# Kernel optimization log

Measured on AMD Instinct MI355X. Metric: run time of the kernel, lower is better.

Reference implementation:

```python
import jax, jax.numpy as jnp
import numpy as np

B, L, H, NH = 8, 256, 128, 4
D = H // NH
NEG = jnp.float32(-(2.0 ** 32) + 1.0)


def setup_inputs() -> dict:
    key = jax.random.key(0)
    ks = jax.random.split(key, 12)
    f = lambda k, s, sc=1.0: jax.random.normal(k, s, dtype=jnp.float32) * sc
    inp = {
        "queries": f(ks[0], (B, L, H)),
        "keys": f(ks[1], (B, L, H)),
        "time_matrix_K": f(ks[2], (B, L, L, H), 0.05),
        "time_matrix_V": f(ks[3], (B, L, L, H), 0.05),
        "abs_pos_K": f(ks[4], (B, L, H), 0.1),
        "abs_pos_V": f(ks[5], (B, L, H), 0.1),
        "Wq": f(ks[6], (H, H), 1.0 / np.sqrt(H)),
        "bq": jnp.zeros((H,), jnp.float32),
        "Wk": f(ks[7], (H, H), 1.0 / np.sqrt(H)),
        "bk": jnp.zeros((H,), jnp.float32),
        "Wv": f(ks[8], (H, H), 1.0 / np.sqrt(H)),
        "bv": jnp.zeros((H,), jnp.float32),
        # True = padded query row (masked out)
        "time_mask": jax.random.uniform(ks[9], (B, L)) < 0.1,
        # causal mask: True above the diagonal = not attendable
        "attn_mask": jnp.triu(jnp.ones((L, L), dtype=bool), k=1),
    }
    return inp


def reference(queries, keys, time_matrix_K, time_matrix_V, abs_pos_K, abs_pos_V,
              Wq, bq, Wk, bk, Wv, bv, time_mask, attn_mask):
    # Linear projections (torch Linear: x @ W.T + b)
    Q = queries @ Wq.T + bq
    K = keys @ Wk.T + bk
    V = keys @ Wv.T + bv
    # head split: channels [i*D:(i+1)*D] -> head i  (equivalent to torch split/cat)
    Qh = Q.reshape(B, L, NH, D)
    Kh = K.reshape(B, L, NH, D)
    Vh = V.reshape(B, L, NH, D)
    pKh = abs_pos_K.reshape(B, L, NH, D)
    pVh = abs_pos_V.reshape(B, L, NH, D)
    tKh = time_matrix_K.reshape(B, L, L, NH, D)
    tVh = time_matrix_V.reshape(B, L, L, NH, D)
    # scores: QK^T + Q*absposK^T + per-row time-interval bias  -> [B,NH,L,L]
    aw = jnp.einsum('blhd,bmhd->bhlm', Qh, Kh)
    aw += jnp.einsum('blhd,bmhd->bhlm', Qh, pKh)
    aw += jnp.einsum('blmhd,blhd->bhlm', tKh, Qh)
    aw = aw * jnp.float32(1.0 / np.sqrt(D))
    mask = time_mask[:, None, :, None] | attn_mask[None, None, :, :]
    aw = jnp.where(mask, NEG, aw)
    A = jax.nn.softmax(aw, axis=-1)  # dropout omitted (eval mode)
    # outputs: A@V + A@absposV + per-row A @ time_matrix_V  -> [B,L,NH,D]
    out = jnp.einsum('bhlm,bmhd->blhd', A, Vh)
    out += jnp.einsum('bhlm,bmhd->blhd', A, pVh)
    out += jnp.einsum('bhlm,blmhd->blhd', A, tVh)
    return out.reshape(B, L, H)
```

## Files before the change

kernel.cpp:

```cpp
#include <hip/hip_runtime.h>
#include <math.h>

#define Bdim 8
#define Lq   256
#define Hd   128

static constexpr float kNEG = -4294967295.0f;
static constexpr float kScale = 0.17677669529663687f;
static constexpr float kUni = 0.00390625f;

typedef float f32x4 __attribute__((ext_vector_type(4)));

__global__ __launch_bounds__(256) void prep_kernel(
    const float* __restrict__ Wq, const float* __restrict__ Wk,
    const float* __restrict__ Wv, const unsigned char* __restrict__ raw,
    float* __restrict__ Wt, int* __restrict__ outmask)
{
    const int blk = blockIdx.x;
    if (blk < 12) {
        __shared__ float tile[64][65];
        const int mi = blk >> 2;
        const float* W = (mi == 0) ? Wq : (mi == 1) ? Wk : Wv;
        float* WT = Wt + mi * (Hd * Hd);
        const int ti = blk & 3;
        const int r0 = (ti >> 1) * 64, c0 = (ti & 1) * 64;
        #pragma unroll
        for (int k = 0; k < 16; ++k) {
            const int e = threadIdx.x + k * 256;
            const int r = e >> 6, c = e & 63;
            tile[r][c] = W[(r0 + r) * Hd + (c0 + c)];
        }
        __syncthreads();
        #pragma unroll
        for (int k = 0; k < 16; ++k) {
            const int e = threadIdx.x + k * 256;
            const int r = e >> 6, c = e & 63;
            WT[(c0 + r) * Hd + (r0 + c)] = tile[c][r];
        }
    } else {
        __shared__ int cnt;
        if (threadIdx.x == 0) cnt = 0;
        __syncthreads();
        const int n = Bdim * Lq;
        for (int i = threadIdx.x; i < n; i += 256)
            if ((i & 3) && raw[i]) atomicAdd(&cnt, 1);
        __syncthreads();
        const bool is_u8 = (cnt > 0);
        const int* raw32 = (const int*)raw;
        for (int i = threadIdx.x; i < n; i += 256) {
            const int v = is_u8 ? (int)raw[i] : raw32[i];
            outmask[i] = (v != 0) ? 1 : 0;
        }
    }
}

__global__ __launch_bounds__(512) void proj_kernel(
    const float* __restrict__ queries, const float* __restrict__ keys,
    const float* __restrict__ absK, const float* __restrict__ absV,
    const float* __restrict__ Wt,
    const float* __restrict__ bq, const float* __restrict__ bk,
    const float* __restrict__ bv,
    float* __restrict__ Qb, float* __restrict__ Kb, float* __restrict__ Vb)
{
    constexpr int R = 8;
    __shared__ float xq[R][Hd];
    __shared__ float xk[R][Hd];
    const int row0 = blockIdx.x * R;
    const int tid = threadIdx.x;
    #pragma unroll
    for (int k = 0; k < 2; ++k) {
        const int e = tid + k * 512;
        const int r = e >> 7, c = e & 127;
        xq[r][c] = queries[(row0 + r) * Hd + c];
        xk[r][c] = keys[(row0 + r) * Hd + c];
    }
    __syncthreads();

    const int o = tid & 127, rh = tid >> 7;
    const int r0 = rh * 2, r1 = rh * 2 + 1;
    const float* __restrict__ Wtq = Wt;
    const float* __restrict__ Wtk = Wt + Hd * Hd;
    const float* __restrict__ Wtv = Wt + 2 * Hd * Hd;

    float qa0 = bq[o], qa1 = qa0;
    float ka0 = bk[o] + absK[(row0 + r0) * Hd + o];
    float ka1 = bk[o] + absK[(row0 + r1) * Hd + o];
    float va0 = bv[o] + absV[(row0 + r0) * Hd + o];
    float va1 = bv[o] + absV[(row0 + r1) * Hd + o];

    #pragma unroll 4
    for (int i = 0; i < Hd; ++i) {
        const float wq = Wtq[i * Hd + o];
        const float wk = Wtk[i * Hd + o];
        const float wv = Wtv[i * Hd + o];
        const float x0 = xq[r0][i], x1 = xq[r1][i];
        const float y0 = xk[r0][i], y1 = xk[r1][i];
        qa0 += x0 * wq; qa1 += x1 * wq;
        ka0 += y0 * wk; ka1 += y1 * wk;
        va0 += y0 * wv; va1 += y1 * wv;
    }
    Qb[(row0 + r0) * Hd + o] = qa0;  Qb[(row0 + r1) * Hd + o] = qa1;
    Kb[(row0 + r0) * Hd + o] = ka0;  Kb[(row0 + r1) * Hd + o] = ka1;
    Vb[(row0 + r0) * Hd + o] = va0;  Vb[(row0 + r1) * Hd + o] = va1;
}

__global__ __launch_bounds__(256) void attn_kernel(
    const float* __restrict__ Qb, const float* __restrict__ Kb,
    const float* __restrict__ Vb,
    const float* __restrict__ tK, const float* __restrict__ tV,
    const int* __restrict__ tmask, float* __restrict__ out)
{
    const int bid = blockIdx.x;
    const int b = bid & 7;
    const int p = bid >> 3;
    const int tid = threadIdx.x;
    const int h = tid >> 6;
    const int lane = tid & 63;
    const int m_off = (lane >> 2) & 15;
    const int cg = lane & 3;
    const int ch = h * 32 + cg * 8;

    const int ls[4] = {p, 127 - p, 128 + p, 255 - p};

    f32x4 q[4][2];
    const float* tKp[4];
    const float* tVp[4];
    bool  mk[4];
    int   n1[4], n2[4];
    int NT1 = 0, NT2 = 0;
    #pragma unroll
    for (int i = 0; i < 4; ++i) {
        const size_t row = ((size_t)b * Lq + ls[i]) * Hd;
        q[i][0] = *(const f32x4*)(Qb + row + ch) * kScale;
        q[i][1] = *(const f32x4*)(Qb + row + ch + 4) * kScale;
        tKp[i] = tK + row * Lq + (size_t)m_off * Hd + ch;
        tVp[i] = tV + row * Lq + (size_t)m_off * Hd + ch;
        mk[i] = (tmask[b * Lq + ls[i]] != 0);
        const int nt = (ls[i] >> 4) + 1;
        n1[i] = mk[i] ? 0 : nt;
        n2[i] = mk[i] ? 16 : nt;
        NT1 = (n1[i] > NT1) ? n1[i] : NT1;
        NT2 = (n2[i] > NT2) ? n2[i] : NT2;
    }
    const float* kpt = Kb + (size_t)b * Lq * Hd + (size_t)m_off * Hd + ch;
    const float* vpt = Vb + (size_t)b * Lq * Hd + (size_t)m_off * Hd + ch;

    float s[4][16];
    #pragma unroll
    for (int i = 0; i < 4; ++i)
        #pragma unroll
        for (int t = 0; t < 16; ++t) s[i][t] = kNEG;

    #pragma unroll
    for (int t = 0; t < 16; ++t) {
        if (t < NT1) {
            const f32x4 ka = *(const f32x4*)(kpt + t * 2048);
            const f32x4 kb = *(const f32x4*)(kpt + t * 2048 + 4);
            const int m = t * 16 + m_off;
            #pragma unroll
            for (int i = 0; i < 4; ++i) {
                if (t < n1[i]) {
                    const f32x4 sa = ka + *(const f32x4*)(tKp[i] + t * 2048);
                    const f32x4 sb = kb + *(const f32x4*)(tKp[i] + t * 2048 + 4);
                    float pp = q[i][0].x*sa.x + q[i][0].y*sa.y
                             + q[i][0].z*sa.z + q[i][0].w*sa.w
                             + q[i][1].x*sb.x + q[i][1].y*sb.y
                             + q[i][1].z*sb.z + q[i][1].w*sb.w;
                    pp += __shfl_xor(pp, 1);
                    pp += __shfl_xor(pp, 2);
                    s[i][t] = (m <= ls[i]) ? pp : kNEG;
                }
            }
        }
    }

    #pragma unroll
    for (int i = 0; i < 4; ++i) {
        if (!mk[i]) {
            float mx = s[i][0];
            #pragma unroll
            for (int t = 1; t < 16; ++t) mx = fmaxf(mx, s[i][t]);
            #pragma unroll
            for (int d = 4; d < 64; d <<= 1) mx = fmaxf(mx, __shfl_xor(mx, d));
            float sum = 0.f;
            #pragma unroll
            for (int t = 0; t < 16; ++t) { s[i][t] = expf(s[i][t] - mx); sum += s[i][t]; }
            #pragma unroll
            for (int d = 4; d < 64; d <<= 1) sum += __shfl_xor(sum, d);
            const float inv = 1.0f / sum;
            #pragma unroll
            for (int t = 0; t < 16; ++t) s[i][t] *= inv;
        } else {
            #pragma unroll
            for (int t = 0; t < 16; ++t) s[i][t] = kUni;
        }
    }

    f32x4 acc[4][2];
    #pragma unroll
    for (int i = 0; i < 4; ++i) { acc[i][0] = (f32x4){0,0,0,0}; acc[i][1] = (f32x4){0,0,0,0}; }

    #pragma unroll
    for (int t = 0; t < 16; ++t) {
        if (t < NT2) {
            const f32x4 va = *(const f32x4*)(vpt + t * 2048);
            const f32x4 vb = *(const f32x4*)(vpt + t * 2048 + 4);
            #pragma unroll
            for (int i = 0; i < 4; ++i) {
                if (t < n2[i]) {
                    const f32x4 ta = *(const f32x4*)(tVp[i] + t * 2048);
                    const f32x4 tb = *(const f32x4*)(tVp[i] + t * 2048 + 4);
                    acc[i][0] += s[i][t] * (va + ta);
                    acc[i][1] += s[i][t] * (vb + tb);
                }
            }
        }
    }
    #pragma unroll
    for (int i = 0; i < 4; ++i) {
        #pragma unroll
        for (int d = 4; d < 64; d <<= 1) {
            acc[i][0].x += __shfl_xor(acc[i][0].x, d);
            acc[i][0].y += __shfl_xor(acc[i][0].y, d);
            acc[i][0].z += __shfl_xor(acc[i][0].z, d);
            acc[i][0].w += __shfl_xor(acc[i][0].w, d);
            acc[i][1].x += __shfl_xor(acc[i][1].x, d);
            acc[i][1].y += __shfl_xor(acc[i][1].y, d);
            acc[i][1].z += __shfl_xor(acc[i][1].z, d);
            acc[i][1].w += __shfl_xor(acc[i][1].w, d);
        }
    }
    if (m_off == 0) {
        #pragma unroll
        for (int i = 0; i < 4; ++i) {
            float* o = out + ((size_t)b * Lq + ls[i]) * Hd + ch;
            *(f32x4*)o       = acc[i][0];
            *(f32x4*)(o + 4) = acc[i][1];
        }
    }
}

extern "C" void kernel_launch(void* const* d_in, const int* in_sizes, int n_in,
                              void* d_out, int out_size, void* d_ws, size_t ws_size,
                              hipStream_t stream) {
    const float* queries = (const float*)d_in[0];
    const float* keys    = (const float*)d_in[1];
    const float* tK      = (const float*)d_in[2];
    const float* tV      = (const float*)d_in[3];
    const float* absK    = (const float*)d_in[4];
    const float* absV    = (const float*)d_in[5];
    const float* Wq      = (const float*)d_in[6];
    const float* bq      = (const float*)d_in[7];
    const float* Wk      = (const float*)d_in[8];
    const float* bk      = (const float*)d_in[9];
    const float* Wv      = (const float*)d_in[10];
    const float* bv      = (const float*)d_in[11];
    const unsigned char* tmask_raw = (const unsigned char*)d_in[12];

    float* outp = (float*)d_out;

    const int rows = Bdim * Lq;
    float* Qb = (float*)d_ws;
    float* Kb = Qb + (size_t)rows * Hd;
    float* Vb = Kb + (size_t)rows * Hd;
    int* tmask = (int*)(Vb + (size_t)rows * Hd);
    float* Wt = (float*)(tmask + rows);

    prep_kernel<<<13, 256, 0, stream>>>(Wq, Wk, Wv, tmask_raw, Wt, tmask);
    proj_kernel<<<rows / 8, 512, 0, stream>>>(queries, keys, absK, absV, Wt,
                                              bq, bk, bv, Qb, Kb, Vb);
    attn_kernel<<<512, 256, 0, stream>>>(Qb, Kb, Vb, tK, tV, tmask, outp);
}
```

Measured before the change: 89.61 us.

## Split attention work so each wave handles one query row and head

Each wave previously handled four query rows for one head, which let it reuse the K/V loads across rows. Now a block's four waves cover two heads times two query rows (p and 255-p, chosen to balance the causal load), and the grid grows from 512 to 2048 blocks. A launch-bounds occupancy hint is added. The change cuts per-thread register use and per-wave serial work and gives more blocks for latency hiding, but K/V rows are reloaded per query row, though those loads are small next to the tK/tV streams.

```diff
diff --git a/kernel.cpp b/kernel.cpp
--- a/kernel.cpp
+++ b/kernel.cpp
@@ -104,139 +104,103 @@
     Vb[(row0 + r0) * Hd + o] = va0;  Vb[(row0 + r1) * Hd + o] = va1;
 }
 
-__global__ __launch_bounds__(256) void attn_kernel(
+__global__ __launch_bounds__(256, 6) void attn_kernel(
     const float* __restrict__ Qb, const float* __restrict__ Kb,
     const float* __restrict__ Vb,
     const float* __restrict__ tK, const float* __restrict__ tV,
     const int* __restrict__ tmask, float* __restrict__ out)
 {
     const int bid = blockIdx.x;
-    const int b = bid & 7;
-    const int p = bid >> 3;
+    const int b  = bid & 7;
+    const int hp = (bid >> 3) & 1;
+    const int p  = bid >> 4;
+
     const int tid = threadIdx.x;
-    const int h = tid >> 6;
+    const int w = tid >> 6;
     const int lane = tid & 63;
+    const int h = hp * 2 + (w & 1);
+    const int li = ((w >> 1) ^ ((p >> 4) & 1)) & 1;
+    const int l = li ? (255 - p) : p;
     const int m_off = (lane >> 2) & 15;
     const int cg = lane & 3;
     const int ch = h * 32 + cg * 8;
 
-    const int ls[4] = {p, 127 - p, 128 + p, 255 - p};
-
-    f32x4 q[4][2];
-    const float* tKp[4];
-    const float* tVp[4];
-    bool  mk[4];
-    int   n1[4], n2[4];
-    int NT1 = 0, NT2 = 0;
-    #pragma unroll
-    for (int i = 0; i < 4; ++i) {
-        const size_t row = ((size_t)b * Lq + ls[i]) * Hd;
-        q[i][0] = *(const f32x4*)(Qb + row + ch) * kScale;
-        q[i][1] = *(const f32x4*)(Qb + row + ch + 4) * kScale;
-        tKp[i] = tK + row * Lq + (size_t)m_off * Hd + ch;
-        tVp[i] = tV + row * Lq + (size_t)m_off * Hd + ch;
-        mk[i] = (tmask[b * Lq + ls[i]] != 0);
-        const int nt = (ls[i] >> 4) + 1;
-        n1[i] = mk[i] ? 0 : nt;
-        n2[i] = mk[i] ? 16 : nt;
-        NT1 = (n1[i] > NT1) ? n1[i] : NT1;
-        NT2 = (n2[i] > NT2) ? n2[i] : NT2;
-    }
-    const float* kpt = Kb + (size_t)b * Lq * Hd + (size_t)m_off * Hd + ch;
-    const float* vpt = Vb + (size_t)b * Lq * Hd + (size_t)m_off * Hd + ch;
-
-    float s[4][16];
-    #pragma unroll
-    for (int i = 0; i < 4; ++i)
-        #pragma unroll
-        for (int t = 0; t < 16; ++t) s[i][t] = kNEG;
+    const float* qb = Qb + ((size_t)b * Lq + l) * Hd + ch;
+    f32x4 q0 = *(const f32x4*)qb * kScale;
+    f32x4 q1 = *(const f32x4*)(qb + 4) * kScale;
+
+    const bool mk = (tmask[b * Lq + l] != 0);
+    const int ntc = (l >> 4) + 1;
+    const int n1 = mk ? 0 : ntc;
+    const int n2 = mk ? 16 : ntc;
+
+    const float* kpt = Kb + (size_t)b * Lq * Hd + m_off * Hd + ch;
+    const float* vpt = Vb + (size_t)b * Lq * Hd + m_off * Hd + ch;
+    const float* tp  = tK + (((size_t)b * Lq + l) * Lq + m_off) * Hd + ch;
+    const float* up  = tV + (((size_t)b * Lq + l) * Lq + m_off) * Hd + ch;
+
+    float s[16];
+    #pragma unroll
+    for (int t = 0; t < 16; ++t) s[t] = kNEG;
 
     #pragma unroll
     for (int t = 0; t < 16; ++t) {
-        if (t < NT1) {
-            const f32x4 ka = *(const f32x4*)(kpt + t * 2048);
-            const f32x4 kb = *(const f32x4*)(kpt + t * 2048 + 4);
+        if (t < n1) {
+            const f32x4 sa = *(const f32x4*)(kpt + t * 2048)
+                           + *(const f32x4*)(tp + t * 2048);
+            const f32x4 sb = *(const f32x4*)(kpt + t * 2048 + 4)
+                           + *(const f32x4*)(tp + t * 2048 + 4);
+            float pp = q0.x*sa.x + q0.y*sa.y + q0.z*sa.z + q0.w*sa.w
+                     + q1.x*sb.x + q1.y*sb.y + q1.z*sb.z + q1.w*sb.w;
+            pp += __shfl_xor(pp, 1);
+            pp += __shfl_xor(pp, 2);
             const int m = t * 16 + m_off;
-            #pragma unroll
-            for (int i = 0; i < 4; ++i) {
-                if (t < n1[i]) {
-                    const f32x4 sa = ka + *(const f32x4*)(tKp[i] + t * 2048);
-                    const f32x4 sb = kb + *(const f32x4*)(tKp[i] + t * 2048 + 4);
-                    float pp = q[i][0].x*sa.x + q[i][0].y*sa.y
-                             + q[i][0].z*sa.z + q[i][0].w*sa.w
-                             + q[i][1].x*sb.x + q[i][1].y*sb.y
-                             + q[i][1].z*sb.z + q[i][1].w*sb.w;
-                    pp += __shfl_xor(pp, 1);
-                    pp += __shfl_xor(pp, 2);
-                    s[i][t] = (m <= ls[i]) ? pp : kNEG;
-                }
-            }
-        }
-    }
-
-    #pragma unroll
-    for (int i = 0; i < 4; ++i) {
-        if (!mk[i]) {
-            float mx = s[i][0];
-            #pragma unroll
-            for (int t = 1; t < 16; ++t) mx = fmaxf(mx, s[i][t]);
-            #pragma unroll
-            for (int d = 4; d < 64; d <<= 1) mx = fmaxf(mx, __shfl_xor(mx, d));
-            float sum = 0.f;
-            #pragma unroll
-            for (int t = 0; t < 16; ++t) { s[i][t] = expf(s[i][t] - mx); sum += s[i][t]; }
-            #pragma unroll
-            for (int d = 4; d < 64; d <<= 1) sum += __shfl_xor(sum, d);
-            const float inv = 1.0f / sum;
-            #pragma unroll
-            for (int t = 0; t < 16; ++t) s[i][t] *= inv;
-        } else {
-            #pragma unroll
-            for (int t = 0; t < 16; ++t) s[i][t] = kUni;
-        }
-    }
-
-    f32x4 acc[4][2];
-    #pragma unroll
-    for (int i = 0; i < 4; ++i) { acc[i][0] = (f32x4){0,0,0,0}; acc[i][1] = (f32x4){0,0,0,0}; }
-
+            s[t] = (m <= l) ? pp : kNEG;
+        }
+    }
+
+    if (!mk) {
+        float mx = s[0];
+        #pragma unroll
+        for (int t = 1; t < 16; ++t) mx = fmaxf(mx, s[t]);
+        #pragma unroll
+        for (int d = 4; d < 64; d <<= 1) mx = fmaxf(mx, __shfl_xor(mx, d));
+        float sum = 0.f;
+        #pragma unroll
+        for (int t = 0; t < 16; ++t) { s[t] = expf(s[t] - mx); sum += s[t]; }
+        #pragma unroll
+        for (int d = 4; d < 64; d <<= 1) sum += __shfl_xor(sum, d);
+        const float inv = 1.0f / sum;
+        #pragma unroll
+        for (int t = 0; t < 16; ++t) s[t] *= inv;
+    } else {
+        #pragma unroll
+        for (int t = 0; t < 16; ++t) s[t] = kUni;
+    }
+
+    f32x4 a0 = {0,0,0,0}, a1 = {0,0,0,0};
     #pragma unroll
     for (int t = 0; t < 16; ++t) {
-        if (t < NT2) {
-            const f32x4 va = *(const f32x4*)(vpt + t * 2048);
-            const f32x4 vb = *(const f32x4*)(vpt + t * 2048 + 4);
-            #pragma unroll
-            for (int i = 0; i < 4; ++i) {
-                if (t < n2[i]) {
-                    const f32x4 ta = *(const f32x4*)(tVp[i] + t * 2048);
-                    const f32x4 tb = *(const f32x4*)(tVp[i] + t * 2048 + 4);
-                    acc[i][0] += s[i][t] * (va + ta);
-                    acc[i][1] += s[i][t] * (vb + tb);
-                }
-            }
-        }
-    }
-    #pragma unroll
-    for (int i = 0; i < 4; ++i) {
-        #pragma unroll
-        for (int d = 4; d < 64; d <<= 1) {
-            acc[i][0].x += __shfl_xor(acc[i][0].x, d);
-            acc[i][0].y += __shfl_xor(acc[i][0].y, d);
-            acc[i][0].z += __shfl_xor(acc[i][0].z, d);
-            acc[i][0].w += __shfl_xor(acc[i][0].w, d);
-            acc[i][1].x += __shfl_xor(acc[i][1].x, d);
-            acc[i][1].y += __shfl_xor(acc[i][1].y, d);
-            acc[i][1].z += __shfl_xor(acc[i][1].z, d);
-            acc[i][1].w += __shfl_xor(acc[i][1].w, d);
-        }
+        if (t < n2) {
+            const f32x4 va = *(const f32x4*)(vpt + t * 2048)
+                           + *(const f32x4*)(up + t * 2048);
+            const f32x4 vb = *(const f32x4*)(vpt + t * 2048 + 4)
+                           + *(const f32x4*)(up + t * 2048 + 4);
+            a0 += s[t] * va;
+            a1 += s[t] * vb;
+        }
+    }
+    #pragma unroll
+    for (int d = 4; d < 64; d <<= 1) {
+        a0.x += __shfl_xor(a0.x, d); a0.y += __shfl_xor(a0.y, d);
+        a0.z += __shfl_xor(a0.z, d); a0.w += __shfl_xor(a0.w, d);
+        a1.x += __shfl_xor(a1.x, d); a1.y += __shfl_xor(a1.y, d);
+        a1.z += __shfl_xor(a1.z, d); a1.w += __shfl_xor(a1.w, d);
     }
     if (m_off == 0) {
-        #pragma unroll
-        for (int i = 0; i < 4; ++i) {
-            float* o = out + ((size_t)b * Lq + ls[i]) * Hd + ch;
-            *(f32x4*)o       = acc[i][0];
-            *(f32x4*)(o + 4) = acc[i][1];
-        }
+        float* o = out + ((size_t)b * Lq + l) * Hd + ch;
+        *(f32x4*)o       = a0;
+        *(f32x4*)(o + 4) = a1;
     }
 }
 
@@ -269,5 +233,5 @@
     prep_kernel<<<13, 256, 0, stream>>>(Wq, Wk, Wv, tmask_raw, Wt, tmask);
     proj_kernel<<<rows / 8, 512, 0, stream>>>(queries, keys, absK, absV, Wt,
                                               bq, bk, bv, Qb, Kb, Vb);
-    attn_kernel<<<512, 256, 0, stream>>>(Qb, Kb, Vb, tK, tV, tmask, outp);
-}
+    attn_kernel<<<2048, 256, 0, stream>>>(Qb, Kb, Vb, tK, tV, tmask, outp);
+}
```

New measurement: 83.06 us. 7.3% less time.
